# Kernel tuning notes

Measured on AMD Instinct MI355X. Metric: run time of the kernel, lower is better.

Reference implementation:

```python
import jax, jax.numpy as jnp
import numpy as np

N, E, IN, H, OUT = 100000, 1600000, 128, 128, 64


def setup_inputs() -> dict:
    key = jax.random.key(0)
    ks = jax.random.split(key, 6)
    glorot = lambda k, i, o: jax.random.normal(k, (i, o), jnp.float32) * np.float32(np.sqrt(2.0 / (i + o)))
    return dict(
        x=jax.random.normal(ks[0], (N, IN), jnp.float32),
        edge_index=jax.random.randint(ks[1], (2, E), 0, N, dtype=jnp.int64 if jax.config.jax_enable_x64 else jnp.int32),
        W1=glorot(ks[2], IN, H), b1=jnp.zeros((H,), jnp.float32),
        W2=glorot(ks[3], H, H), b2=jnp.zeros((H,), jnp.float32),
        W3=glorot(ks[4], H, OUT), b3=jnp.zeros((OUT,), jnp.float32),
    )


def _gcn_norm(edge_index, num_nodes):
    # add self loops with weight 1.0 (GCNConv add_self_loops=True, edge_weight=None -> ones)
    loop = jnp.arange(num_nodes, dtype=edge_index.dtype)
    src = jnp.concatenate([edge_index[0], loop])
    dst = jnp.concatenate([edge_index[1], loop])
    ew = jnp.ones(src.shape, jnp.float32)
    deg = jax.ops.segment_sum(ew, dst, num_segments=num_nodes)  # in-degree on dst
    dinv = jnp.where(deg > 0, jax.lax.rsqrt(deg), 0.0)
    norm = dinv[src] * ew * dinv[dst]  # [E+N]
    return src, dst, norm


def _conv(x, src, dst, norm, W, b):
    h = x @ W                                        # linear transform first (GCNConv order)
    msg = h[src] * norm[:, None]                     # gather + scale, [E+N, F]
    agg = jax.ops.segment_sum(msg, dst, num_segments=x.shape[0])  # scatter-add
    return agg + b


def reference(x, edge_index, W1, b1, W2, b2, W3, b3):
    # eval-mode forward: dropout is identity
    src, dst, norm = _gcn_norm(edge_index, x.shape[0])  # same graph -> norm shared across layers
    h = jax.nn.relu(_conv(x, src, dst, norm, W1, b1))
    h = jax.nn.relu(_conv(h, src, dst, norm, W2, b2))
    h = _conv(h, src, dst, norm, W3, b3)
    return jax.nn.log_softmax(h, axis=-1)
```

## Files before the change

### kernel.cpp

```cpp
#include <hip/hip_runtime.h>

typedef unsigned int u32;
typedef unsigned short u16;
typedef unsigned char u8;
typedef long i64;
typedef __attribute__((ext_vector_type(8))) short short8;
typedef __attribute__((ext_vector_type(4))) float f32x4;

#define MAXBIN 1024
#define SORT_TPB 1024
#define BINCAP 4096
#define CSRCAP 5120

__device__ inline u16 f2bf(float f) {
    u32 u = __builtin_bit_cast(u32, f);
    u32 r = (u + 0x7fffu + ((u >> 16) & 1u)) >> 16;
    return (u16)r;
}

__device__ inline f32x4 mfma_fp8(uint2 a, uint2 b, f32x4 c) {
    return __builtin_amdgcn_mfma_f32_16x16x32_fp8_fp8(
        __builtin_bit_cast(i64, a), __builtin_bit_cast(i64, b), c, 0, 0, 0);
}

__device__ inline int permP(int p) {
    return ((p >> 5) << 5) + ((p & 3) << 3) + ((p >> 2) & 7);
}

__global__ __launch_bounds__(SORT_TPB) void k_bscatter(const int* __restrict__ ei, int E, int W,
                                                       int* __restrict__ binCnt,
                                                       u32* __restrict__ binned, int NBIN) {
    __shared__ int lh[MAXBIN];
    __shared__ int lb[MAXBIN];
    int tid = threadIdx.x;
    for (int i = tid; i < NBIN; i += SORT_TPB) lh[i] = 0;
    __syncthreads();
    int s = blockIdx.x * W, e = min(E, s + W);
    for (int j = s + tid; j < e; j += SORT_TPB) atomicAdd(&lh[ei[E + j] >> 7], 1);
    __syncthreads();
    for (int i = tid; i < NBIN; i += SORT_TPB) {
        int h = lh[i];
        int base = 0;
        if (h) {
            base = atomicAdd(&binCnt[i], h);
            if (base + h > BINCAP) base = BINCAP - h;
        }
        lb[i] = i * BINCAP + base;
    }
    __syncthreads();
    for (int i = tid; i < NBIN; i += SORT_TPB) lh[i] = 0;
    __syncthreads();
    for (int j = s + tid; j < e; j += SORT_TPB) {
        int d = ei[E + j];
        int b = d >> 7;
        int r = atomicAdd(&lh[b], 1);
        binned[lb[b] + r] = ((u32)ei[j] << 7) | (u32)(d & 127);
    }
}

__global__ __launch_bounds__(256) void k_bcsr(const u32* __restrict__ binned,
                                              const int* __restrict__ binCnt,
                                              int N, int* __restrict__ offs,
                                              int* __restrict__ ends,
                                              float* __restrict__ dinv,
                                              int* __restrict__ csr) {
    __shared__ int cnt[128];
    __shared__ int off[128];
    __shared__ int tot;
    __shared__ int fillEnd;
    int b = blockIdx.x;
    int tid = threadIdx.x;
    int dLo = b << 7;
    int nd = min(128, N - dLo);
    int bbase = b * BINCAP;
    int gCnt = min(binCnt[b], BINCAP);
    int pbase = b * CSRCAP;
    if (tid < 128) cnt[tid] = 0;
    __syncthreads();
    for (int j = tid; j < gCnt; j += 256) atomicAdd(&cnt[binned[bbase + j] & 127u], 1);
    __syncthreads();
    int c = (tid < 128) ? cnt[tid] : 0;
    int pc = (tid < 128) ? ((c + 8) & ~7) : 0;
    int lane = tid & 63;
    int isc = pc;
    for (int d = 1; d < 64; d <<= 1) { int o = __shfl_up(isc, d, 64); if (lane >= d) isc += o; }
    if (tid == 63) tot = isc;
    __syncthreads();
    int add = (tid >= 64 && tid < 128) ? tot : 0;
    if (tid < 128) off[tid] = add + isc - pc;
    if (tid == 127) fillEnd = add + isc;
    __syncthreads();
    for (int j = tid; j < fillEnd; j += 256) csr[pbase + j] = N;
    __syncthreads();
    if (tid < nd) {
        offs[dLo + tid] = pbase + off[tid];
        ends[dLo + tid] = pbase + off[tid] + pc;
        dinv[dLo + tid] = rsqrtf((float)(c + 1));
        csr[pbase + off[tid] + c] = dLo + tid;
    }
    if (tid < 128) cnt[tid] = 0;
    __syncthreads();
    for (int j = tid; j < gCnt; j += 256) {
        u32 v = binned[bbase + j];
        int d7 = (int)(v & 127u);
        int r = atomicAdd(&cnt[d7], 1);
        csr[pbase + off[d7] + r] = (int)(v >> 7);
    }
}

__global__ void k_wtall(const float* __restrict__ W1, const float* __restrict__ W2,
                        const float* __restrict__ W3, u16* __restrict__ wt1,
                        u16* __restrict__ wt2, u16* __restrict__ wt3) {
    int idx = blockIdx.x * 256 + threadIdx.x;
    if (idx < 16384) {
        int k = idx >> 7, m = idx & 127;
        wt1[m * 128 + k] = f2bf(W1[idx]);
    } else if (idx < 32768) {
        int i = idx - 16384, p = i >> 7, m = i & 127;
        wt2[m * 128 + p] = f2bf(W2[permP(p) * 128 + m]);
    } else if (idx < 40960) {
        int i = idx - 32768, p = i >> 6, m = i & 63;
        wt3[m * 128 + p] = f2bf(W3[permP(p) * 64 + m]);
    }
}

template <int M, bool F32IN>
__global__ __launch_bounds__(256) void k_gemm(const void* __restrict__ xin,
                                              const u16* __restrict__ wt,
                                              const float* __restrict__ dinv,
                                              u8* __restrict__ g8, int N) {
    constexpr int K = 128;
    constexpr int LDK = 136;
    __shared__ u16 lwt[M * LDK];
    int tid = threadIdx.x;
    if (blockIdx.x == 0 && tid < M / 16)
        *(uint4*)(g8 + (size_t)N * M + (size_t)tid * 16) = make_uint4(0u, 0u, 0u, 0u);
    const uint4* wsrc = (const uint4*)wt;
#pragma unroll
    for (int c = tid; c < M * K / 8; c += 256) {
        int row = c >> 4, kc = c & 15;
        *(uint4*)&lwt[row * LDK + kc * 8] = wsrc[c];
    }
    __syncthreads();
    int lane = tid & 63, wv = tid >> 6;
    int node = blockIdx.x * 64 + wv * 16 + (lane & 15);
    int nodec = min(node, N - 1);
    int kr = (lane >> 4) * 8;
    f32x4 acc[M / 16];
#pragma unroll
    for (int t = 0; t < M / 16; t++) acc[t] = (f32x4){0.f, 0.f, 0.f, 0.f};
#pragma unroll
    for (int ks = 0; ks < 4; ks++) {
        short8 bfr;
        if (F32IN) {
            const float* xr = (const float*)xin + (size_t)nodec * K + ks * 32 + kr;
            float4 fa = *(const float4*)xr;
            float4 fb = *(const float4*)(xr + 4);
            bfr = (short8){(short)f2bf(fa.x), (short)f2bf(fa.y), (short)f2bf(fa.z),
                           (short)f2bf(fa.w), (short)f2bf(fb.x), (short)f2bf(fb.y),
                           (short)f2bf(fb.z), (short)f2bf(fb.w)};
        } else {
            bfr = *(const short8*)((const u16*)xin + (size_t)nodec * K + ks * 32 + kr);
        }
#pragma unroll
        for (int t = 0; t < M / 16; t++) {
            short8 afr = *(const short8*)&lwt[(t * 16 + (lane & 15)) * LDK + ks * 32 + kr];
            acc[t] = __builtin_amdgcn_mfma_f32_16x16x32_bf16(afr, bfr, acc[t], 0, 0, 0);
        }
    }
    if (node < N) {
        float dv16 = dinv[node] * 16.0f;
        int r0 = (lane >> 4) * 4;
#pragma unroll
        for (int t = 0; t < M / 16; t++) {
            u32 w = __builtin_amdgcn_cvt_pk_fp8_f32(acc[t][0] * dv16, acc[t][1] * dv16, 0, false);
            w = __builtin_amdgcn_cvt_pk_fp8_f32(acc[t][2] * dv16, acc[t][3] * dv16, w, true);
            *(u32*)(g8 + (size_t)node * M + t * 16 + r0) = w;
        }
    }
}

__global__ __launch_bounds__(256) void k_agg128(const u8* __restrict__ g8,
                                                const int* __restrict__ offs,
                                                const int* __restrict__ ends,
                                                const int* __restrict__ csr,
                                                const float* __restrict__ dinv,
                                                const float* __restrict__ bias,
                                                u16* __restrict__ hout, int N) {
    int wid = (blockIdx.x * 256 + threadIdx.x) >> 6;
    if (wid >= N) return;
    int lane = threadIdx.x & 63;
    int q = lane >> 4;
    int f = lane & 15;
    int s = offs[wid], e = ends[wid];
    uint2 bsel;
    bsel.x = (f < 4) ? (0x38u << (8 * f)) : 0u;
    bsel.y = (f >= 4 && f < 8) ? (0x38u << (8 * (f - 4))) : 0u;
    const u8* gf = g8 + f * 8;
    f32x4 ac0 = {0.f, 0.f, 0.f, 0.f}, ac1 = ac0, ac2 = ac0, ac3 = ac0;
    int j = s;
    int i0 = csr[j + q];
    int i1 = csr[j + 4 + q];
    int i2 = csr[j + 8 + q];
    int i3 = csr[j + 12 + q];
    for (; j + 16 <= e; j += 16) {
        uint2 w0 = *(const uint2*)(gf + ((u32)i0 << 7));
        uint2 w1 = *(const uint2*)(gf + ((u32)i1 << 7));
        uint2 w2 = *(const uint2*)(gf + ((u32)i2 << 7));
        uint2 w3 = *(const uint2*)(gf + ((u32)i3 << 7));
        i0 = csr[j + 16 + q];
        i1 = csr[j + 20 + q];
        i2 = csr[j + 24 + q];
        i3 = csr[j + 28 + q];
        ac0 = mfma_fp8(w0, bsel, ac0);
        ac1 = mfma_fp8(w1, bsel, ac1);
        ac2 = mfma_fp8(w2, bsel, ac2);
        ac3 = mfma_fp8(w3, bsel, ac3);
    }
    if (j < e) {
        uint2 w0 = *(const uint2*)(gf + ((u32)i0 << 7));
        uint2 w1 = *(const uint2*)(gf + ((u32)i1 << 7));
        ac0 = mfma_fp8(w0, bsel, ac0);
        ac1 = mfma_fp8(w1, bsel, ac1);
    }
    f32x4 a = (ac0 + ac1) + (ac2 + ac3);
    int jn = lane & 15, fq = lane >> 4;
    if (jn < 8) {
        float sc = dinv[wid] * 0.0625f;
        u32 o0, o1;
        {
            float v0 = fmaxf(fmaf(a[0], sc, bias[(4 * fq + 0) * 8 + jn]), 0.f);
            float v1 = fmaxf(fmaf(a[1], sc, bias[(4 * fq + 1) * 8 + jn]), 0.f);
            o0 = (u32)f2bf(v0) | ((u32)f2bf(v1) << 16);
        }
        {
            float v2 = fmaxf(fmaf(a[2], sc, bias[(4 * fq + 2) * 8 + jn]), 0.f);
            float v3 = fmaxf(fmaf(a[3], sc, bias[(4 * fq + 3) * 8 + jn]), 0.f);
            o1 = (u32)f2bf(v2) | ((u32)f2bf(v3) << 16);
        }
        *(uint2*)&hout[(size_t)wid * 128 + fq * 32 + jn * 4] = make_uint2(o0, o1);
    }
}

__global__ __launch_bounds__(256) void k_agg64(const u8* __restrict__ g8,
                                               const int* __restrict__ offs,
                                               const int* __restrict__ ends,
                                               const int* __restrict__ csr,
                                               const float* __restrict__ dinv,
                                               const float* __restrict__ bias,
                                               float* __restrict__ out, int N) {
    __shared__ float sm[4][64];
    int wid = (blockIdx.x * 256 + threadIdx.x) >> 6;
    if (wid >= N) return;
    int lane = threadIdx.x & 63;
    int wv = (int)(threadIdx.x >> 6);
    int q = lane >> 4;
    int f = lane & 15;
    int qq = q + ((f >> 3) << 2);
    int s = offs[wid], e = ends[wid];
    uint2 bsel;
    bsel.x = (f < 4) ? (0x38u << (8 * f)) : 0u;
    bsel.y = (f >= 4 && f < 8) ? (0x38u << (8 * (f - 4))) : 0u;
    const u8* gf = g8 + (f & 7) * 8;
    f32x4 ac0 = {0.f, 0.f, 0.f, 0.f}, ac1 = ac0;
    int j = s;
    int iA = csr[j + qq];
    int iB = csr[j + 8 + qq];
    for (; j + 16 <= e; j += 16) {
        uint2 wA = *(const uint2*)(gf + ((u32)iA << 6));
        uint2 wB = *(const uint2*)(gf + ((u32)iB << 6));
        iA = csr[j + 16 + qq];
        iB = csr[j + 24 + qq];
        ac0 = mfma_fp8(wA, bsel, ac0);
        ac1 = mfma_fp8(wB, bsel, ac1);
    }
    if (j < e) {
        uint2 wA = *(const uint2*)(gf + ((u32)iA << 6));
        ac0 = mfma_fp8(wA, bsel, ac0);
    }
    f32x4 a = ac0 + ac1;
#pragma unroll
    for (int r = 0; r < 4; r++) a[r] += __shfl_xor(a[r], 32, 64);
    int jn = lane & 15, fq = lane >> 4;
    bool act = (jn < 8) && (fq < 2);
    if (act) {
        float sc = dinv[wid] * 0.0625f;
        float v0 = fmaf(a[0], sc, bias[(4 * fq + 0) * 8 + jn]);
        float v1 = fmaf(a[1], sc, bias[(4 * fq + 1) * 8 + jn]);
        float v2 = fmaf(a[2], sc, bias[(4 * fq + 2) * 8 + jn]);
        float v3 = fmaf(a[3], sc, bias[(4 * fq + 3) * 8 + jn]);
        float m = fmaxf(fmaxf(v0, v1), fmaxf(v2, v3));
        m = fmaxf(m, __shfl_xor(m, 1, 64));
        m = fmaxf(m, __shfl_xor(m, 2, 64));
        m = fmaxf(m, __shfl_xor(m, 4, 64));
        m = fmaxf(m, __shfl_xor(m, 16, 64));
        float ss = __expf(v0 - m) + __expf(v1 - m) + __expf(v2 - m) + __expf(v3 - m);
        ss += __shfl_xor(ss, 1, 64);
        ss += __shfl_xor(ss, 2, 64);
        ss += __shfl_xor(ss, 4, 64);
        ss += __shfl_xor(ss, 16, 64);
        float lg = m + __logf(ss);
        sm[wv][(4 * fq + 0) * 8 + jn] = v0 - lg;
        sm[wv][(4 * fq + 1) * 8 + jn] = v1 - lg;
        sm[wv][(4 * fq + 2) * 8 + jn] = v2 - lg;
        sm[wv][(4 * fq + 3) * 8 + jn] = v3 - lg;
    }
    if (lane < 16) {
        float4 ov = *(float4*)&sm[wv][lane * 4];
        *(float4*)&out[(size_t)wid * 64 + lane * 4] = ov;
    }
}

extern "C" void kernel_launch(void* const* d_in, const int* in_sizes, int n_in,
                              void* d_out, int out_size, void* d_ws, size_t ws_size,
                              hipStream_t stream) {
    const float* x  = (const float*)d_in[0];
    const int*   ei = (const int*)d_in[1];
    const float* W1 = (const float*)d_in[2];
    const float* b1 = (const float*)d_in[3];
    const float* W2 = (const float*)d_in[4];
    const float* b2 = (const float*)d_in[5];
    const float* W3 = (const float*)d_in[6];
    const float* b3 = (const float*)d_in[7];
    const int N = in_sizes[0] / 128;
    const int E = in_sizes[1] / 2;
    const int NBIN = (N + 127) >> 7;

    char* ws = (char*)d_ws;
    size_t o = 0;
    auto alloc = [&](size_t bytes) -> char* {
        char* p = ws + o;
        o += (bytes + 255) & ~(size_t)255;
        return p;
    };
    int*   binCnt = (int*)alloc((size_t)MAXBIN * 4);
    float* dinv   = (float*)alloc((size_t)N * 4);
    int*   offs   = (int*)alloc((size_t)N * 4);
    int*   endsA  = (int*)alloc((size_t)N * 4);
    int*   csr    = (int*)alloc(((size_t)NBIN * CSRCAP + 64) * 4);
    u16*   wt1    = (u16*)alloc(128 * 128 * 2);
    u16*   wt2    = (u16*)alloc(128 * 128 * 2);
    u16*   wt3    = (u16*)alloc(64 * 128 * 2);
    u8*    g8     = (u8*)alloc(((size_t)N + 1) * 128);
    u16*   hbuf   = (u16*)alloc((size_t)N * 128 * 2);
    u32*   binned = (u32*)hbuf;
    float* outp   = (float*)d_out;

    hipMemsetAsync(binCnt, 0, (size_t)MAXBIN * 4, stream);
    int W256 = (E + 255) / 256;
    k_bscatter<<<256, SORT_TPB, 0, stream>>>(ei, E, W256, binCnt, binned, NBIN);
    k_bcsr<<<NBIN, 256, 0, stream>>>(binned, binCnt, N, offs, endsA, dinv, csr);
    k_wtall<<<(40960 + 255) / 256, 256, 0, stream>>>(W1, W2, W3, wt1, wt2, wt3);

    int gG = (N + 63) / 64;
    int gA = (int)(((size_t)N * 64 + 255) / 256);

    k_gemm<128, true ><<<gG, 256, 0, stream>>>(x,    wt1, dinv, g8, N);
    k_agg128<<<gA, 256, 0, stream>>>(g8, offs, endsA, csr, dinv, b1, hbuf, N);
    k_gemm<128, false><<<gG, 256, 0, stream>>>(hbuf, wt2, dinv, g8, N);
    k_agg128<<<gA, 256, 0, stream>>>(g8, offs, endsA, csr, dinv, b2, hbuf, N);
    k_gemm<64,  false><<<gG, 256, 0, stream>>>(hbuf, wt3, dinv, g8, N);
    k_agg64<<<gA, 256, 0, stream>>>(g8, offs, endsA, csr, dinv, b3, outp, N);
}
```

Measured before the change: 288.8 us.

## Aggregate two nodes per wavefront in MFMA-based gather kernels

Each wavefront in the aggregation kernels now handles two destination nodes at once. The lanes are split between the two nodes' edge lists, and the MFMA B-selector routes each half into separate output columns. The intent is to fill MFMA columns that were previously wasted and to halve the wave count. In exchange the loop runs until the longer of the two edge lists finishes, inactive slots are padded with a zero row at index N, and the software prefetch of the next CSR indices is dropped, which may expose more load latency.

```diff
diff --git a/kernel.cpp b/kernel.cpp
--- a/kernel.cpp
+++ b/kernel.cpp
@@ -187,58 +187,65 @@
                                                 const float* __restrict__ dinv,
                                                 const float* __restrict__ bias,
                                                 u16* __restrict__ hout, int N) {
-    int wid = (blockIdx.x * 256 + threadIdx.x) >> 6;
-    if (wid >= N) return;
+    int wp = (blockIdx.x * 256 + threadIdx.x) >> 6;
+    int widA = wp * 2;
+    if (widA >= N) return;
+    int widB = widA + 1;
+    bool hasB = widB < N;
     int lane = threadIdx.x & 63;
     int q = lane >> 4;
     int f = lane & 15;
-    int s = offs[wid], e = ends[wid];
+    int sA = offs[widA], eA = ends[widA];
+    int sB = hasB ? offs[widB] : 0;
+    int eB = hasB ? ends[widB] : 0;
+    int nn = f & 7;
+    bool on = (f < 8) ? (q < 2) : (q >= 2);
     uint2 bsel;
-    bsel.x = (f < 4) ? (0x38u << (8 * f)) : 0u;
-    bsel.y = (f >= 4 && f < 8) ? (0x38u << (8 * (f - 4))) : 0u;
+    bsel.x = (on && nn < 4) ? (0x38u << (8 * nn)) : 0u;
+    bsel.y = (on && nn >= 4) ? (0x38u << (8 * (nn - 4))) : 0u;
     const u8* gf = g8 + f * 8;
+    bool isA = (q < 2);
+    int qm = q & 1;
     f32x4 ac0 = {0.f, 0.f, 0.f, 0.f}, ac1 = ac0, ac2 = ac0, ac3 = ac0;
-    int j = s;
-    int i0 = csr[j + q];
-    int i1 = csr[j + 4 + q];
-    int i2 = csr[j + 8 + q];
-    int i3 = csr[j + 12 + q];
-    for (; j + 16 <= e; j += 16) {
+    int jA = sA, jB = sB;
+    while (jA < eA || jB < eB) {
+        bool okA = jA < eA, okB = jB < eB;
+        int base = isA ? jA : jB;
+        bool ok = isA ? okA : okB;
+        int i0 = csr[base + qm];
+        int i1 = csr[base + 2 + qm];
+        int i2 = csr[base + 4 + qm];
+        int i3 = csr[base + 6 + qm];
+        if (!ok) { i0 = N; i1 = N; i2 = N; i3 = N; }
         uint2 w0 = *(const uint2*)(gf + ((u32)i0 << 7));
         uint2 w1 = *(const uint2*)(gf + ((u32)i1 << 7));
         uint2 w2 = *(const uint2*)(gf + ((u32)i2 << 7));
         uint2 w3 = *(const uint2*)(gf + ((u32)i3 << 7));
-        i0 = csr[j + 16 + q];
-        i1 = csr[j + 20 + q];
-        i2 = csr[j + 24 + q];
-        i3 = csr[j + 28 + q];
         ac0 = mfma_fp8(w0, bsel, ac0);
         ac1 = mfma_fp8(w1, bsel, ac1);
         ac2 = mfma_fp8(w2, bsel, ac2);
         ac3 = mfma_fp8(w3, bsel, ac3);
-    }
-    if (j < e) {
-        uint2 w0 = *(const uint2*)(gf + ((u32)i0 << 7));
-        uint2 w1 = *(const uint2*)(gf + ((u32)i1 << 7));
-        ac0 = mfma_fp8(w0, bsel, ac0);
-        ac1 = mfma_fp8(w1, bsel, ac1);
+        if (okA) jA += 8;
+        if (okB) jB += 8;
     }
     f32x4 a = (ac0 + ac1) + (ac2 + ac3);
     int jn = lane & 15, fq = lane >> 4;
-    if (jn < 8) {
-        float sc = dinv[wid] * 0.0625f;
+    int node = (jn < 8) ? widA : widB;
+    if (node < N) {
+        float sc = dinv[node] * 0.0625f;
+        int bb = (jn & 7);
         u32 o0, o1;
         {
-            float v0 = fmaxf(fmaf(a[0], sc, bias[(4 * fq + 0) * 8 + jn]), 0.f);
-            float v1 = fmaxf(fmaf(a[1], sc, bias[(4 * fq + 1) * 8 + jn]), 0.f);
+            float v0 = fmaxf(fmaf(a[0], sc, bias[(4 * fq + 0) * 8 + bb]), 0.f);
+            float v1 = fmaxf(fmaf(a[1], sc, bias[(4 * fq + 1) * 8 + bb]), 0.f);
             o0 = (u32)f2bf(v0) | ((u32)f2bf(v1) << 16);
         }
         {
-            float v2 = fmaxf(fmaf(a[2], sc, bias[(4 * fq + 2) * 8 + jn]), 0.f);
-            float v3 = fmaxf(fmaf(a[3], sc, bias[(4 * fq + 3) * 8 + jn]), 0.f);
+            float v2 = fmaxf(fmaf(a[2], sc, bias[(4 * fq + 2) * 8 + bb]), 0.f);
+            float v3 = fmaxf(fmaf(a[3], sc, bias[(4 * fq + 3) * 8 + bb]), 0.f);
             o1 = (u32)f2bf(v2) | ((u32)f2bf(v3) << 16);
         }
-        *(uint2*)&hout[(size_t)wid * 128 + fq * 32 + jn * 4] = make_uint2(o0, o1);
+        *(uint2*)&hout[(size_t)node * 128 + fq * 32 + bb * 4] = make_uint2(o0, o1);
     }
 }
 
@@ -249,46 +256,52 @@
                                                const float* __restrict__ dinv,
                                                const float* __restrict__ bias,
                                                float* __restrict__ out, int N) {
-    __shared__ float sm[4][64];
-    int wid = (blockIdx.x * 256 + threadIdx.x) >> 6;
-    if (wid >= N) return;
+    __shared__ float sm[4][2][64];
+    int wp = (blockIdx.x * 256 + threadIdx.x) >> 6;
+    int widA = wp * 2;
+    if (widA >= N) return;
+    int widB = widA + 1;
+    bool hasB = widB < N;
     int lane = threadIdx.x & 63;
     int wv = (int)(threadIdx.x >> 6);
     int q = lane >> 4;
     int f = lane & 15;
-    int qq = q + ((f >> 3) << 2);
-    int s = offs[wid], e = ends[wid];
+    bool isA = (f < 8);
+    int sA = offs[widA], eA = ends[widA];
+    int sB = hasB ? offs[widB] : 0;
+    int eB = hasB ? ends[widB] : 0;
     uint2 bsel;
     bsel.x = (f < 4) ? (0x38u << (8 * f)) : 0u;
     bsel.y = (f >= 4 && f < 8) ? (0x38u << (8 * (f - 4))) : 0u;
     const u8* gf = g8 + (f & 7) * 8;
     f32x4 ac0 = {0.f, 0.f, 0.f, 0.f}, ac1 = ac0;
-    int j = s;
-    int iA = csr[j + qq];
-    int iB = csr[j + 8 + qq];
-    for (; j + 16 <= e; j += 16) {
-        uint2 wA = *(const uint2*)(gf + ((u32)iA << 6));
-        uint2 wB = *(const uint2*)(gf + ((u32)iB << 6));
-        iA = csr[j + 16 + qq];
-        iB = csr[j + 24 + qq];
-        ac0 = mfma_fp8(wA, bsel, ac0);
-        ac1 = mfma_fp8(wB, bsel, ac1);
-    }
-    if (j < e) {
-        uint2 wA = *(const uint2*)(gf + ((u32)iA << 6));
-        ac0 = mfma_fp8(wA, bsel, ac0);
+    int jA = sA, jB = sB;
+    while (jA < eA || jB < eB) {
+        bool okA = jA < eA, okB = jB < eB;
+        int base = isA ? jA : jB;
+        bool ok = isA ? okA : okB;
+        int i0 = csr[base + q];
+        int i1 = csr[base + 4 + q];
+        if (!ok) { i0 = N; i1 = N; }
+        uint2 w0 = *(const uint2*)(gf + ((u32)i0 << 6));
+        uint2 w1 = *(const uint2*)(gf + ((u32)i1 << 6));
+        ac0 = mfma_fp8(w0, bsel, ac0);
+        ac1 = mfma_fp8(w1, bsel, ac1);
+        if (okA) jA += 8;
+        if (okB) jB += 8;
     }
     f32x4 a = ac0 + ac1;
-#pragma unroll
-    for (int r = 0; r < 4; r++) a[r] += __shfl_xor(a[r], 32, 64);
     int jn = lane & 15, fq = lane >> 4;
-    bool act = (jn < 8) && (fq < 2);
+    int half = fq >> 1;
+    int node = widA + half;
+    bool act = (jn < 8) && (node < N);
     if (act) {
-        float sc = dinv[wid] * 0.0625f;
-        float v0 = fmaf(a[0], sc, bias[(4 * fq + 0) * 8 + jn]);
-        float v1 = fmaf(a[1], sc, bias[(4 * fq + 1) * 8 + jn]);
-        float v2 = fmaf(a[2], sc, bias[(4 * fq + 2) * 8 + jn]);
-        float v3 = fmaf(a[3], sc, bias[(4 * fq + 3) * 8 + jn]);
+        float sc = dinv[node] * 0.0625f;
+        int ch = (fq & 1);
+        float v0 = fmaf(a[0], sc, bias[(4 * ch + 0) * 8 + jn]);
+        float v1 = fmaf(a[1], sc, bias[(4 * ch + 1) * 8 + jn]);
+        float v2 = fmaf(a[2], sc, bias[(4 * ch + 2) * 8 + jn]);
+        float v3 = fmaf(a[3], sc, bias[(4 * ch + 3) * 8 + jn]);
         float m = fmaxf(fmaxf(v0, v1), fmaxf(v2, v3));
         m = fmaxf(m, __shfl_xor(m, 1, 64));
         m = fmaxf(m, __shfl_xor(m, 2, 64));
@@ -300,14 +313,18 @@
         ss += __shfl_xor(ss, 4, 64);
         ss += __shfl_xor(ss, 16, 64);
         float lg = m + __logf(ss);
-        sm[wv][(4 * fq + 0) * 8 + jn] = v0 - lg;
-        sm[wv][(4 * fq + 1) * 8 + jn] = v1 - lg;
-        sm[wv][(4 * fq + 2) * 8 + jn] = v2 - lg;
-        sm[wv][(4 * fq + 3) * 8 + jn] = v3 - lg;
-    }
-    if (lane < 16) {
-        float4 ov = *(float4*)&sm[wv][lane * 4];
-        *(float4*)&out[(size_t)wid * 64 + lane * 4] = ov;
+        sm[wv][half][(4 * ch + 0) * 8 + jn] = v0 - lg;
+        sm[wv][half][(4 * ch + 1) * 8 + jn] = v1 - lg;
+        sm[wv][half][(4 * ch + 2) * 8 + jn] = v2 - lg;
+        sm[wv][half][(4 * ch + 3) * 8 + jn] = v3 - lg;
+    }
+    if (lane < 32) {
+        int h = lane >> 4;
+        int node2 = widA + h;
+        if (node2 < N) {
+            float4 ov = *(float4*)&sm[wv][h][(lane & 15) * 4];
+            *(float4*)&out[(size_t)node2 * 64 + (lane & 15) * 4] = ov;
+        }
     }
 }
 
@@ -353,7 +370,8 @@
     k_wtall<<<(40960 + 255) / 256, 256, 0, stream>>>(W1, W2, W3, wt1, wt2, wt3);
 
     int gG = (N + 63) / 64;
-    int gA = (int)(((size_t)N * 64 + 255) / 256);
+    int P  = (N + 1) / 2;
+    int gA = (P + 3) / 4;
 
     k_gemm<128, true ><<<gG, 256, 0, stream>>>(x,    wt1, dinv, g8, N);
     k_agg128<<<gA, 256, 0, stream>>>(g8, offs, endsA, csr, dinv, b1, hbuf, N);
```

New measurement: 277.8 us. 1.04x faster.
